# Optimization experiments

Measured on AMD Instinct MI355X. Metric: run time of the kernel, lower is better.

The kernel has to match this reference:

```python
import jax, jax.numpy as jnp
import numpy as np

EPS = 1e-12  # F.normalize default eps
SCALE = 8 * 56  # magic denominator from the original code


def setup_inputs() -> dict:
    key = jax.random.key(0)
    B, C, K = 256, 2048, 4
    P = B // K  # 64 identities
    k1, k2 = jax.random.split(key)
    inputs = jax.random.normal(k1, (B, C), dtype=jnp.float32)
    # PK-sampled batch: P identities, each with K=4 consecutive samples
    targets = jnp.repeat(jnp.arange(P, dtype=jnp.int32), K)
    # binary modality label (visible / infrared)
    subs = jax.random.randint(k2, (B,), 0, 2, dtype=jnp.int32)
    return {"inputs": inputs, "targets": targets, "subs": subs}


def reference(inputs, targets, subs):
    B, C = inputs.shape
    # centers[i] = mean of samples sharing identity targets[4*i]
    center_t = targets[::4]                                  # (P,)
    cmask = (targets[None, :] == center_t[:, None]).astype(inputs.dtype)  # (P, B)
    centers = (cmask @ inputs) / cmask.sum(-1, keepdims=True)             # (P, C)

    id_mask = targets[None, :] == targets[:, None]           # (B, B) bool
    # modality_mask = subs[None,:] == subs[:,None]  # computed but unused in original

    def per_center(c):
        vec = inputs - c                                     # (B, C)
        vec = vec / jnp.maximum(
            jnp.linalg.norm(vec, axis=-1, keepdims=True), EPS)
        angle = vec @ vec.T                                  # (B, B) cosine angles
        # min over positives per row (each row has exactly 4 positives)
        pos = jnp.where(id_mask, angle, jnp.inf).min(axis=-1)            # (B,)
        # max over clamp(angle, 0) on negatives per row
        neg = jnp.where(id_mask, 0.0, jnp.maximum(angle, 0.0)).max(axis=-1)
        # matmul(exp(-pos).T, exp(neg)) is a (1,1) dot product; .mean() is identity
        return jnp.sum(jnp.exp(-pos) * jnp.exp(neg)) / SCALE

    losses = jax.vmap(per_center)(centers)                   # (P,)
    # NOTE: original returns `loss` (the LAST iteration's loss), not the
    # accumulated `losses` — we reproduce that behavior faithfully.
    return losses[-1]
```

## Files before the change

kernel.cpp:

```cpp
#include <hip/hip_runtime.h>
#include <math.h>

#define BN 256
#define CN 2048
#define C4 512
#define EPSF 1e-12f

__global__ __launch_bounds__(256, 1) void gram_kernel(const float* __restrict__ in,
                                                      float* __restrict__ D,
                                                      float* __restrict__ s_pre,
                                                      float* __restrict__ out) {
    const int b    = blockIdx.x;
    const int tid  = threadIdx.x;
    const int lane = tid & 63;
    const int wave = tid >> 6;
    const bool odd1 = (lane & 1);
    const bool odd2 = (lane & 2);

    if (b == 0 && tid == 0) out[0] = 0.f;

    __shared__ float s_ctr[16];

    const float4* __restrict__ in4 = (const float4*)in;

    float4 a[4][8];
    int cur_ib = -1;

    const int u0 = 9 * b;
    for (int k = 0; k < 9; ++k) {
        const int u = u0 + k;
        const int t = u >> 3;
        const int s = u & 7;
        int jb = 0;
        jb += (t >= 8);   jb += (t >= 24);  jb += (t >= 48);  jb += (t >= 80);
        jb += (t >= 120); jb += (t >= 168); jb += (t >= 224);
        const int ib = t - 4 * jb * (jb + 1);
        const int i0 = ib * 4;

        if (ib != cur_ib) {
            cur_ib = ib;
#pragma unroll
            for (int r = 0; r < 4; ++r)
#pragma unroll
                for (int tt = 0; tt < 8; ++tt)
                    a[r][tt] = in4[(i0 + r) * C4 + lane + 64 * tt];
        }

        const int j = 32 * jb + wave + 4 * s;
        float4 bv[8];
#pragma unroll
        for (int tt = 0; tt < 8; ++tt)
            bv[tt] = in4[j * C4 + lane + 64 * tt];

        float a0 = 0.f, a1 = 0.f, a2 = 0.f, a3 = 0.f;
#pragma unroll
        for (int tt = 0; tt < 8; ++tt) {
            const float4 b4 = bv[tt];
            a0 += a[0][tt].x * b4.x + a[0][tt].y * b4.y + a[0][tt].z * b4.z + a[0][tt].w * b4.w;
            a1 += a[1][tt].x * b4.x + a[1][tt].y * b4.y + a[1][tt].z * b4.z + a[1][tt].w * b4.w;
            a2 += a[2][tt].x * b4.x + a[2][tt].y * b4.y + a[2][tt].z * b4.z + a[2][tt].w * b4.w;
            a3 += a[3][tt].x * b4.x + a[3][tt].y * b4.y + a[3][tt].z * b4.z + a[3][tt].w * b4.w;
        }

        const float c01 = (odd1 ? a1 : a0) + __shfl_xor(odd1 ? a0 : a1, 1, 64);
        const float c23 = (odd1 ? a3 : a2) + __shfl_xor(odd1 ? a2 : a3, 1, 64);
        float c = (odd2 ? c23 : c01) + __shfl_xor(odd2 ? c01 : c23, 2, 64);
        c += __shfl_xor(c, 4, 64);
        c += __shfl_xor(c, 8, 64);
        c += __shfl_xor(c, 16, 64);
        c += __shfl_xor(c, 32, 64);

        if (lane < 4) {
            const int i = i0 + lane;
            D[i * BN + j] = c;
            D[j * BN + i] = c;
            if (jb == 7 && s == 7)
                s_ctr[wave * 4 + lane] = c;
        }

        if (jb == 7 && s == 7) {
            __syncthreads();
            if (tid < 4) {
                const float sp = (((s_ctr[tid] + s_ctr[4 + tid]) + s_ctr[8 + tid])
                                  + s_ctr[12 + tid]) * 0.25f;
                s_pre[i0 + tid] = sp;
            }
            __syncthreads();
        }
    }
}

__global__ __launch_bounds__(256) void finish_kernel(const float* __restrict__ D,
                                                     const float* __restrict__ s_pre,
                                                     const int* __restrict__ targets,
                                                     float* __restrict__ out) {
    const int tid = threadIdx.x;
    const int blk = blockIdx.x;

    __shared__ int   s_t[BN];
    __shared__ float s_s[BN];
    __shared__ float s_inv[BN];
    __shared__ float s_red[4];

    const int row = blk * 32 + (tid >> 3);
    const int sub = tid & 7;

    const float4* __restrict__ D4 = (const float4*)D;
    float4 drow[8];
#pragma unroll
    for (int q = 0; q < 8; ++q)
        drow[q] = D4[row * (BN / 4) + q * 8 + sub];

    const int   t_own = targets[tid];
    const float dii   = D[tid * BN + tid];
    const float si    = s_pre[tid];
    const int   ti    = targets[row];
    const float diiR  = D[row * BN + row];
    const float siR   = s_pre[row];
    const float sp0   = s_pre[BN - 4];
    const float sp1   = s_pre[BN - 3];
    const float sp2   = s_pre[BN - 2];
    const float sp3   = s_pre[BN - 1];

    const float cc = (((sp0 + sp1) + sp2) + sp3) * 0.25f;

    const float nrm2 = fmaxf(dii - 2.f * si + cc, 0.f);
    const float inv  = 1.0f / fmaxf(sqrtf(nrm2), EPSF);
    const float nrm2R = fmaxf(diiR - 2.f * siR + cc, 0.f);
    const float invR  = 1.0f / fmaxf(sqrtf(nrm2R), EPSF);

    s_t[tid]   = t_own;
    s_s[tid]   = si;
    s_inv[tid] = inv;
    __syncthreads();

    float pos = INFINITY;
    float neg = 0.f;
#pragma unroll
    for (int q = 0; q < 8; ++q) {
        const float4 d = drow[q];
        const int j = 4 * (q * 8 + sub);
        const float g0 = (d.x - siR - s_s[j + 0] + cc) * invR * s_inv[j + 0];
        const float g1 = (d.y - siR - s_s[j + 1] + cc) * invR * s_inv[j + 1];
        const float g2 = (d.z - siR - s_s[j + 2] + cc) * invR * s_inv[j + 2];
        const float g3 = (d.w - siR - s_s[j + 3] + cc) * invR * s_inv[j + 3];
        if (s_t[j + 0] == ti) pos = fminf(pos, g0); else neg = fmaxf(neg, fmaxf(g0, 0.f));
        if (s_t[j + 1] == ti) pos = fminf(pos, g1); else neg = fmaxf(neg, fmaxf(g1, 0.f));
        if (s_t[j + 2] == ti) pos = fminf(pos, g2); else neg = fmaxf(neg, fmaxf(g2, 0.f));
        if (s_t[j + 3] == ti) pos = fminf(pos, g3); else neg = fmaxf(neg, fmaxf(g3, 0.f));
    }
#pragma unroll
    for (int off = 1; off <= 4; off <<= 1) {
        pos = fminf(pos, __shfl_xor(pos, off, 64));
        neg = fmaxf(neg, __shfl_xor(neg, off, 64));
    }
    float val = (sub == 0) ? expf(neg - pos) : 0.f;
#pragma unroll
    for (int off = 1; off <= 32; off <<= 1) val += __shfl_xor(val, off, 64);
    if ((tid & 63) == 0) s_red[tid >> 6] = val;
    __syncthreads();
    if (tid == 0)
        atomicAdd(out, (s_red[0] + s_red[1] + s_red[2] + s_red[3]) * (1.0f / 448.0f));
}

extern "C" void kernel_launch(void* const* d_in, const int* in_sizes, int n_in,
                              void* d_out, int out_size, void* d_ws, size_t ws_size,
                              hipStream_t stream) {
    const float* in      = (const float*)d_in[0];
    const int*   targets = (const int*)d_in[1];

    float* D     = (float*)d_ws;
    float* s_pre = D + BN * BN;
    float* out   = (float*)d_out;

    gram_kernel  <<<256, 256, 0, stream>>>(in, D, s_pre, out);
    finish_kernel<<<8,   256, 0, stream>>>(D, s_pre, targets, out);
}
```

Measured before the change: 72.94 us.

## Redistribute Gram tile work across 384 blocks with split tail tiles

Instead of each of 256 blocks processing 9 consecutive work units (which can straddle row-block boundaries and reload the A rows), blocks now own one row-block tile. The first 256 tiles are done whole (8 units each), and the remaining 32 tiles are split into 4 blocks of 2 units. This removes mid-loop A reloads and per-iteration tile index math, and uses 384 blocks to fill more CUs. The trade-off is load imbalance between 8-unit and 2-unit blocks and redundant A loads in the split tiles.

```diff
diff --git a/kernel.cpp b/kernel.cpp
--- a/kernel.cpp
+++ b/kernel.cpp
@@ -5,6 +5,47 @@
 #define CN 2048
 #define C4 512
 #define EPSF 1e-12f
+
+__device__ __forceinline__ void gram_unit(const float4* __restrict__ in4,
+                                          const float4 (&a)[4][8],
+                                          float* __restrict__ D,
+                                          float* __restrict__ s_ctr,
+                                          const int i0, const int j0,
+                                          const int jb, const int s,
+                                          const int lane, const int wave,
+                                          const bool odd1, const bool odd2) {
+    const int j = j0 + wave + 4 * s;
+    float4 bv[8];
+#pragma unroll
+    for (int tt = 0; tt < 8; ++tt)
+        bv[tt] = in4[j * C4 + lane + 64 * tt];
+
+    float a0 = 0.f, a1 = 0.f, a2 = 0.f, a3 = 0.f;
+#pragma unroll
+    for (int tt = 0; tt < 8; ++tt) {
+        const float4 b4 = bv[tt];
+        a0 += a[0][tt].x * b4.x + a[0][tt].y * b4.y + a[0][tt].z * b4.z + a[0][tt].w * b4.w;
+        a1 += a[1][tt].x * b4.x + a[1][tt].y * b4.y + a[1][tt].z * b4.z + a[1][tt].w * b4.w;
+        a2 += a[2][tt].x * b4.x + a[2][tt].y * b4.y + a[2][tt].z * b4.z + a[2][tt].w * b4.w;
+        a3 += a[3][tt].x * b4.x + a[3][tt].y * b4.y + a[3][tt].z * b4.z + a[3][tt].w * b4.w;
+    }
+
+    const float c01 = (odd1 ? a1 : a0) + __shfl_xor(odd1 ? a0 : a1, 1, 64);
+    const float c23 = (odd1 ? a3 : a2) + __shfl_xor(odd1 ? a2 : a3, 1, 64);
+    float c = (odd2 ? c23 : c01) + __shfl_xor(odd2 ? c01 : c23, 2, 64);
+    c += __shfl_xor(c, 4, 64);
+    c += __shfl_xor(c, 8, 64);
+    c += __shfl_xor(c, 16, 64);
+    c += __shfl_xor(c, 32, 64);
+
+    if (lane < 4) {
+        const int i = i0 + lane;
+        D[i * BN + j] = c;
+        D[j * BN + i] = c;
+        if (jb == 7 && s == 7)
+            s_ctr[wave * 4 + lane] = c;
+    }
+}
 
 __global__ __launch_bounds__(256, 1) void gram_kernel(const float* __restrict__ in,
                                                       float* __restrict__ D,
@@ -19,73 +60,42 @@
 
     if (b == 0 && tid == 0) out[0] = 0.f;
 
+    int t, s_lo;
+    if (b < 256) { t = b;                      s_lo = 0; }
+    else         { t = 256 + ((b - 256) >> 2); s_lo = ((b - 256) & 3) << 1; }
+    int jb = 0;
+    jb += (t >= 8);   jb += (t >= 24);  jb += (t >= 48);  jb += (t >= 80);
+    jb += (t >= 120); jb += (t >= 168); jb += (t >= 224);
+    const int ib = t - 4 * jb * (jb + 1);
+    const int i0 = ib * 4;
+    const int j0 = jb * 32;
+
     __shared__ float s_ctr[16];
 
     const float4* __restrict__ in4 = (const float4*)in;
 
     float4 a[4][8];
-    int cur_ib = -1;
-
-    const int u0 = 9 * b;
-    for (int k = 0; k < 9; ++k) {
-        const int u = u0 + k;
-        const int t = u >> 3;
-        const int s = u & 7;
-        int jb = 0;
-        jb += (t >= 8);   jb += (t >= 24);  jb += (t >= 48);  jb += (t >= 80);
-        jb += (t >= 120); jb += (t >= 168); jb += (t >= 224);
-        const int ib = t - 4 * jb * (jb + 1);
-        const int i0 = ib * 4;
-
-        if (ib != cur_ib) {
-            cur_ib = ib;
 #pragma unroll
-            for (int r = 0; r < 4; ++r)
-#pragma unroll
-                for (int tt = 0; tt < 8; ++tt)
-                    a[r][tt] = in4[(i0 + r) * C4 + lane + 64 * tt];
-        }
-
-        const int j = 32 * jb + wave + 4 * s;
-        float4 bv[8];
+    for (int r = 0; r < 4; ++r)
 #pragma unroll
         for (int tt = 0; tt < 8; ++tt)
-            bv[tt] = in4[j * C4 + lane + 64 * tt];
+            a[r][tt] = in4[(i0 + r) * C4 + lane + 64 * tt];
 
-        float a0 = 0.f, a1 = 0.f, a2 = 0.f, a3 = 0.f;
-#pragma unroll
-        for (int tt = 0; tt < 8; ++tt) {
-            const float4 b4 = bv[tt];
-            a0 += a[0][tt].x * b4.x + a[0][tt].y * b4.y + a[0][tt].z * b4.z + a[0][tt].w * b4.w;
-            a1 += a[1][tt].x * b4.x + a[1][tt].y * b4.y + a[1][tt].z * b4.z + a[1][tt].w * b4.w;
-            a2 += a[2][tt].x * b4.x + a[2][tt].y * b4.y + a[2][tt].z * b4.z + a[2][tt].w * b4.w;
-            a3 += a[3][tt].x * b4.x + a[3][tt].y * b4.y + a[3][tt].z * b4.z + a[3][tt].w * b4.w;
-        }
+    if (b < 256) {
+#pragma unroll 2
+        for (int s = 0; s < 8; ++s)
+            gram_unit(in4, a, D, s_ctr, i0, j0, jb, s, lane, wave, odd1, odd2);
+    } else {
+        gram_unit(in4, a, D, s_ctr, i0, j0, jb, s_lo,     lane, wave, odd1, odd2);
+        gram_unit(in4, a, D, s_ctr, i0, j0, jb, s_lo + 1, lane, wave, odd1, odd2);
+    }
 
-        const float c01 = (odd1 ? a1 : a0) + __shfl_xor(odd1 ? a0 : a1, 1, 64);
-        const float c23 = (odd1 ? a3 : a2) + __shfl_xor(odd1 ? a2 : a3, 1, 64);
-        float c = (odd2 ? c23 : c01) + __shfl_xor(odd2 ? c01 : c23, 2, 64);
-        c += __shfl_xor(c, 4, 64);
-        c += __shfl_xor(c, 8, 64);
-        c += __shfl_xor(c, 16, 64);
-        c += __shfl_xor(c, 32, 64);
-
-        if (lane < 4) {
-            const int i = i0 + lane;
-            D[i * BN + j] = c;
-            D[j * BN + i] = c;
-            if (jb == 7 && s == 7)
-                s_ctr[wave * 4 + lane] = c;
-        }
-
-        if (jb == 7 && s == 7) {
-            __syncthreads();
-            if (tid < 4) {
-                const float sp = (((s_ctr[tid] + s_ctr[4 + tid]) + s_ctr[8 + tid])
-                                  + s_ctr[12 + tid]) * 0.25f;
-                s_pre[i0 + tid] = sp;
-            }
-            __syncthreads();
+    if (jb == 7 && (b < 256 || s_lo == 6)) {
+        __syncthreads();
+        if (tid < 4) {
+            const float sp = (((s_ctr[tid] + s_ctr[4 + tid]) + s_ctr[8 + tid])
+                              + s_ctr[12 + tid]) * 0.25f;
+            s_pre[i0 + tid] = sp;
         }
     }
 }
@@ -173,6 +183,6 @@
     float* s_pre = D + BN * BN;
     float* out   = (float*)d_out;
 
-    gram_kernel  <<<256, 256, 0, stream>>>(in, D, s_pre, out);
+    gram_kernel  <<<384, 256, 0, stream>>>(in, D, s_pre, out);
     finish_kernel<<<8,   256, 0, stream>>>(D, s_pre, targets, out);
 }
```

New measurement: 72.64 us. No clear change (-0.4%).
